# Optimization experiments

Hardware: AMD Instinct MI355X
Metric: run time of the kernel (lower is better)

## Reference

```python
import jax, jax.numpy as jnp
import numpy as np


def _gru_cell(x, h, W_ih, W_hh, b_ih, b_hh):
    # torch.nn.GRUCell semantics, gate order (r, z, n)
    gi = x @ W_ih.T + b_ih          # [B, 3H]
    gh = h @ W_hh.T + b_hh          # [B, 3H]
    ir, iz, inn = jnp.split(gi, 3, axis=-1)
    hr, hz, hn = jnp.split(gh, 3, axis=-1)
    r = jax.nn.sigmoid(ir + hr)
    z = jax.nn.sigmoid(iz + hz)
    n = jnp.tanh(inn + r * hn)
    return (1.0 - z) * n + z * h


def setup_inputs() -> dict:
    key = jax.random.key(0)
    ks = jax.random.split(key, 9)
    B, T, X, H = 128, 512, 64, 256
    s = 0.05
    return {
        "input": jax.random.normal(ks[0], (B, T, X), jnp.float32),
        "h_enc": jax.random.normal(ks[1], (B, H), jnp.float32),
        "W_ih": jax.random.normal(ks[2], (3 * H, X), jnp.float32) * s,
        "W_hh": jax.random.normal(ks[3], (3 * H, H), jnp.float32) * s,
        "b_ih": jnp.zeros((3 * H,), jnp.float32),
        "b_hh": jnp.zeros((3 * H,), jnp.float32),
        "W_out": jax.random.normal(ks[4], (X, H), jnp.float32) * s,
        "b_out": jnp.zeros((X,), jnp.float32),
        "mask0": jax.random.randint(ks[5], (T,), 0, 2, jnp.int32),
        "mask1": jax.random.randint(ks[6], (T,), 0, 2, jnp.int32),
        "skip_size": 4,
    }


def _skip_tables(T, skip):
    # Replicates Python-list negative indexing of the original forward.
    # Skip-list position at the GRU call (pre-append):  2i   if i<skip else i-skip
    # Skip-list position at the projection (post-append): 2i+1 if i<skip else i-skip
    # Positions < skip are zero placeholders; position p >= skip is H[p-skip].
    g_idx = np.zeros(T, np.int32); g_zero = np.zeros(T, bool)
    p_idx = np.zeros(T, np.int32); p_zero = np.zeros(T, bool)
    for i in range(T):
        pg = 2 * i if i < skip else i - skip
        pp = 2 * i + 1 if i < skip else i - skip
        g_zero[i] = pg < skip; g_idx[i] = max(pg - skip, 0)
        p_zero[i] = pp < skip; p_idx[i] = max(pp - skip, 0)
    return g_idx, g_zero, p_idx, p_zero


def reference(input, h_enc, W_ih, W_hh, b_ih, b_hh, W_out, b_out, mask0, mask1, skip_size):
    B, T, X = input.shape
    H = h_enc.shape[1]
    g_idx, g_zero, p_idx, p_zero = _skip_tables(T, int(skip_size))
    m0 = mask0.astype(input.dtype)
    m1 = mask1.astype(input.dtype)

    xs = (jnp.arange(T), m0, m1,
          jnp.asarray(g_idx), jnp.asarray(g_zero),
          jnp.asarray(p_idx), jnp.asarray(p_zero))

    def step(carry, sx):
        h_prev, x_prev, buf = carry          # buf: [T, B, H] history of GRU outputs
        i, a0, a1, gi, gz, pi, pz = sx
        skip_g = jnp.where(gz, 0.0, buf[gi])            # [B, H]
        hidden = h_prev * a0 + skip_g * a1
        h_new = _gru_cell(x_prev, hidden, W_ih, W_hh, b_ih, b_hh)
        buf = buf.at[i].set(h_new)                       # append H[i]
        skip_p = jnp.where(pz, 0.0, buf[pi])
        out = (h_prev + skip_p) @ W_out.T + b_out        # [B, X]
        return (h_new, out, buf), out

    buf0 = jnp.zeros((T, B, H), input.dtype)
    go = jnp.zeros((B, X), input.dtype)                  # GO token
    (_, _, _), outs = jax.lax.scan(step, (h_enc, go, buf0), xs)
    return jnp.transpose(outs, (1, 0, 2))                # [B, T, X]
```

## Files before the change

### kernel.cpp

```cpp
#include <hip/hip_runtime.h>

typedef _Float16 h2_t __attribute__((ext_vector_type(2)));

constexpr int T_ = 512;
constexpr int X_ = 64;
constexpr int H_ = 256;
constexpr int NWG = 128;
constexpr int NT = 512;
constexpr int RS = 16;

constexpr int G_TOTAL = 64 * NT;

__device__ __forceinline__ float sigmoid_f(float x) {
  float e = __expf(fminf(-x, 80.f));
  return 1.f / (1.f + e);
}
__device__ __forceinline__ float tanh_f(float x) {
  float e = __expf(fminf(-2.f * x, 80.f));
  return (1.f - e) / (1.f + e);
}

__device__ __forceinline__ unsigned pk2(float a, float b) {
  h2_t v;
  v[0] = (_Float16)a;
  v[1] = (_Float16)b;
  return __builtin_bit_cast(unsigned, v);
}
__device__ __forceinline__ uint4 pk8(const float* s) {
  return make_uint4(pk2(s[0], s[1]), pk2(s[2], s[3]), pk2(s[4], s[5]),
                    pk2(s[6], s[7]));
}

__device__ __forceinline__ float dotp(unsigned w, unsigned h, float acc) {
  h2_t wv = __builtin_bit_cast(h2_t, w);
  h2_t hv = __builtin_bit_cast(h2_t, h);
#if __has_builtin(__builtin_amdgcn_fdot2)
  return __builtin_amdgcn_fdot2(wv, hv, acc, false);
#else
  acc = fmaf((float)wv[0], (float)hv[0], acc);
  return fmaf((float)wv[1], (float)hv[1], acc);
#endif
}
__device__ __forceinline__ float dotq(uint4 w, uint4 h, float acc) {
  acc = dotp(w.x, h.x, acc);
  acc = dotp(w.y, h.y, acc);
  acc = dotp(w.z, h.z, acc);
  acc = dotp(w.w, h.w, acc);
  return acc;
}

__device__ __forceinline__ float dpp_xor1(float x) {
  int v = __builtin_amdgcn_update_dpp(0, __builtin_bit_cast(int, x), 0xB1,
                                      0xF, 0xF, true);
  return __builtin_bit_cast(float, v);
}
__device__ __forceinline__ float dpp_xor2(float x) {
  int v = __builtin_amdgcn_update_dpp(0, __builtin_bit_cast(int, x), 0x4E,
                                      0xF, 0xF, true);
  return __builtin_bit_cast(float, v);
}

__device__ __forceinline__ void bar_lds() {
  asm volatile("s_waitcnt lgkmcnt(0)\n\ts_barrier" ::: "memory");
}

__global__ void prep_kernel(const float* __restrict__ Wih,
                            const float* __restrict__ Whh,
                            const float* __restrict__ Wout,
                            uint4* __restrict__ G) {
  int id = blockIdx.x * 256 + threadIdx.x;
  if (id >= G_TOTAL) return;
  int t = id & (NT - 1), u = id >> 9;
  int c = t >> 1, kh = t & 1;
  if (u < 32) {
    int g = u >> 4, j = u & 15;
    G[id] = pk8(Whh + (size_t)(g * 256 + c) * H_ + kh * 128 + j * 8);
  } else if (u < 48) {
    int j = u - 32;
    G[id] = pk8(Whh + (size_t)(512 + c) * H_ + kh * 128 + j * 8);
  } else if (u < 60) {
    int v = u - 48, g = v >> 2, j = v & 3;
    G[id] = pk8(Wih + (size_t)(g * 256 + c) * X_ + kh * 32 + j * 8);
  } else {
    int j = u - 60, xc = t >> 3, sl = t & 7;
    G[id] = pk8(Wout + (size_t)xc * H_ + sl * 32 + j * 8);
  }
}

#define PTW(cp) (((cp) >> 4) * 36 + ((cp)&15))
#define HIW(w) ((w) + (((w) >> 6) << 2))


#define GATES(p, i, hn)                                                      \
  float hn;                                                                  \
  {                                                                          \
    float a0 = 0, a1 = 0, z0 = 0, z1 = 0, n0 = 0, n1 = 0, ni = 0;            \
    const uint4* h4 = ((const uint4*)hid2[p]) + kh * 17;                     \
    _Pragma("unroll") for (int j = 0; j < 16; j += 2) {                      \
      uint4 ha = h4[j], hb = h4[j + 1];       \
      uint4 wna = wn4[j * NT + t], wnb = wn4[(j + 1) * NT + t];              \
      a0 = dotq(whh_rz[j], ha, a0);                                          \
      a1 = dotq(whh_rz[j + 1], hb, a1);                                      \
      z0 = dotq(whh_rz[16 + j], ha, z0);                                     \
      z1 = dotq(whh_rz[17 + j], hb, z1);                                     \
      n0 = dotq(wna, ha, n0);                                                \
      n1 = dotq(wnb, hb, n1);                                                \
    }                                                                        \
    const uint4* x4 = ((const uint4*)xt2[p]) + kh * 4;                       \
    _Pragma("unroll") for (int j = 0; j < 4; ++j) {                          \
      uint4 xa = x4[j];                                                      \
      a0 = dotq(wih[j], xa, a0);                                             \
      z0 = dotq(wih[4 + j], xa, z0);                                         \
      ni = dotq(wih[8 + j], xa, ni);                                         \
    }                                                                        \
    float ar = a0 + a1, az = z0 + z1, anh = n0 + n1;                         \
    ar += dpp_xor1(ar);                                                      \
    az += dpp_xor1(az);                                                      \
    anh += dpp_xor1(anh);                                                    \
    ni += dpp_xor1(ni);                                                      \
    float r = sigmoid_f(ar + bsr);                                           \
    float z = sigmoid_f(az + bsz);                                           \
    float n = tanh_f(ni + bin_ + r * (anh + bhn_));                          \
    hn = fmaf(z, hid_reg - n, n);                    \
    if (kh == 0) ring[(i) & (RS - 1)][c] = hn;                               \
  }

#define PROJ_FIN(q, i)                                                       \
  {                                                                          \
    fa += dpp_xor1(fa);                                                      \
    fa += dpp_xor2(fa);                                                      \
    fa += __shfl_xor(fa, 4);                                                 \
    float o = fa + bo;                                                       \
    if (sl == 0) out[ob + (size_t)(i)*X_ + xc] = o;                          \
    float oo = __shfl_xor(o, 8);                                             \
    if ((t & 15) == 0) xt2[q][t >> 4] = pk2(o, oo);                          \
  }

#define PROJ(p, q, i)                                                        \
  {                                                                          \
    float fa = 0;                                                            \
    const uint4* p4 = (const uint4*)&pt2[p][sl * 36];                        \
    _Pragma("unroll") for (int j = 0; j < 4; ++j) fa =                       \
        dotq(wout[j], p4[j], fa);                                            \
    PROJ_FIN(q, i)                                                           \
  }

#define MSTEP(i, p, q)                                                       \
  {                                                                          \
    float fa = 0;                                                            \
    const uint4* p4 = (const uint4*)&pt2[p][sl * 36];                        \
    _Pragma("unroll") for (int j = 0; j < 4; ++j) fa =                       \
        dotq(wout[j], p4[j], fa);                                            \
    GATES(p, i, hn)                                                          \
    PROJ_FIN(q, i)                                                           \
    if ((i) + 1 < T_) {                                                      \
      float sgp = ring[((i) + 1 - 2 * skip) & (RS - 1)][c];                  \
      float hidn = m0f[(i) + 1] * hn + m1f[(i) + 1] * sgp;                   \
      float ptn = hn + sgp;                                                  \
      hid_reg = hidn;                                                        \
      float ho = dpp_xor2(hidn);                                             \
      float po = dpp_xor2(ptn);                                              \
      if ((t & 3) == 0) {                                                    \
        int w = t >> 2;                                                      \
        hid2[q][HIW(w)] = pk2(hidn, ho);                                     \
        pt2[q][PTW(w)] = pk2(ptn, po);                                       \
      }                                                                      \
    }                                                                        \
    bar_lds();                                                               \
  }

__global__ __attribute__((amdgpu_flat_work_group_size(NT, NT),
                          amdgpu_waves_per_eu(2, 2))) void decoder_kernel(
    const float* __restrict__ h_enc, const float* __restrict__ b_ih,
    const float* __restrict__ b_hh, const float* __restrict__ b_out,
    const int* __restrict__ mask0, const int* __restrict__ mask1,
    const int* __restrict__ skipp, const uint4* __restrict__ G,
    float* __restrict__ out) {
  __shared__ alignas(16) uint4 wn4[16 * NT];
  __shared__ float ring[RS][H_];
  __shared__ alignas(16) unsigned hid2[2][136];
  __shared__ alignas(16) unsigned pt2[2][8 * 36];
  __shared__ alignas(16) unsigned xt2[2][X_ / 2];
  __shared__ float m0f[T_], m1f[T_];

  const int t = threadIdx.x;
  const int b = blockIdx.x;
  const int c = t >> 1, kh = t & 1;
  const int xc = t >> 3, sl = t & 7;
  const size_t ob = (size_t)b * T_ * X_;

  uint4 whh_rz[32];
  uint4 wih[12];
  uint4 wout[4];
#pragma unroll
  for (int u = 0; u < 32; ++u) whh_rz[u] = G[u * NT + t];
#pragma unroll
  for (int u = 0; u < 12; ++u) wih[u] = G[(48 + u) * NT + t];
#pragma unroll
  for (int u = 0; u < 4; ++u) wout[u] = G[(60 + u) * NT + t];

#pragma unroll
  for (int u = 0; u < 16; ++u) wn4[u * NT + t] = G[(32 + u) * NT + t];
  m0f[t] = (float)mask0[t];
  m1f[t] = (float)mask1[t];

  const int skip = skipp[0];
  const int i0 = (skip == 0) ? T_ : ((2 * skip < T_) ? 2 * skip : T_);

  const float bsr = b_ih[c] + b_hh[c];
  const float bsz = b_ih[H_ + c] + b_hh[H_ + c];
  const float bin_ = b_ih[2 * H_ + c];
  const float bhn_ = b_hh[2 * H_ + c];
  const float bo = b_out[xc];

  float hp = h_enc[(size_t)b * H_ + c];
  float hid_reg = (float)mask0[0] * hp;
  float hps_reg = hp;
  {
    float ho = dpp_xor2(hid_reg);
    if ((t & 3) == 0) hid2[0][HIW(t >> 2)] = pk2(hid_reg, ho);
  }
  if (t < X_ / 2) xt2[0][t] = 0u;
  __syncthreads();

  for (int i = 0; i < i0; ++i) {
    const int p = i & 1, q = p ^ 1;
    GATES(p, i, hn)
    {
      int ppos = (i < skip) ? 2 * i + 1 : i - skip;
      bool pz = ppos < skip;
      int pi = ppos - skip;
      if (pi < 0) pi = 0;
      float sp = pz ? 0.f : ((pi == i) ? hn : ring[pi & (RS - 1)][c]);
      float ptv = hps_reg + sp;
      float po = dpp_xor2(ptv);
      if ((t & 3) == 0) pt2[p][PTW(t >> 2)] = pk2(ptv, po);
    }
    if (i + 1 < T_) {
      int i1 = i + 1;
      int pg = (i1 < skip) ? 2 * i1 : i1 - skip;
      bool gz = pg < skip;
      int gi = pg - skip;
      if (gi < 0) gi = 0;
      if (gi >= i1) gz = true;
      float sg = gz ? 0.f : ((gi == i) ? hn : ring[gi & (RS - 1)][c]);
      float hidn = m0f[i1] * hn + m1f[i1] * sg;
      hid_reg = hidn;
      float ho = dpp_xor2(hidn);
      if ((t & 3) == 0) hid2[q][HIW(t >> 2)] = pk2(hidn, ho);
      if (skip > 0 && i1 >= 2 * skip) {
        float sgp = ring[(i1 - 2 * skip) & (RS - 1)][c];
        float ptn = hn + sgp;
        float po2 = dpp_xor2(ptn);
        if ((t & 3) == 0) pt2[q][PTW(t >> 2)] = pk2(ptn, po2);
      }
    }
    hps_reg = hn;
    __syncthreads();
    PROJ(p, q, i)
    __syncthreads();
  }

#pragma unroll 1
  for (int i = i0; i < T_; i += 2) {
    MSTEP(i, 0, 1)
    MSTEP(i + 1, 1, 0)
  }
}

extern "C" void kernel_launch(void* const* d_in, const int* in_sizes, int n_in,
                              void* d_out, int out_size, void* d_ws,
                              size_t ws_size, hipStream_t stream) {
  (void)in_sizes; (void)n_in; (void)out_size; (void)ws_size;
  const float* h_enc = (const float*)d_in[1];
  const float* W_ih = (const float*)d_in[2];
  const float* W_hh = (const float*)d_in[3];
  const float* b_ih = (const float*)d_in[4];
  const float* b_hh = (const float*)d_in[5];
  const float* W_out = (const float*)d_in[6];
  const float* b_out = (const float*)d_in[7];
  const int* mask0 = (const int*)d_in[8];
  const int* mask1 = (const int*)d_in[9];
  const int* skipp = (const int*)d_in[10];
  float* out = (float*)d_out;
  uint4* G = (uint4*)d_ws;

  prep_kernel<<<dim3(G_TOTAL / 256), dim3(256), 0, stream>>>(W_ih, W_hh,
                                                             W_out, G);
  decoder_kernel<<<dim3(NWG), dim3(NT), 0, stream>>>(
      h_enc, b_ih, b_hh, b_out, mask0, mask1, skipp, G, out);
}
```

Baseline: 1.077 ms.

## Remap GRU work so each thread quad computes two hidden columns

Each group of four threads now owns two adjacent hidden columns and splits K four ways, instead of each pair of threads owning one column with K split two ways. The weight packing, the LDS layouts for hidden, x and projection vectors, and the reductions change to match. The packed fp16 pairs are now two columns from one thread, so the dpp exchange before LDS writes goes away and each hidden vector load feeds six dot chains. The cost is an extra dpp step in each reduction, eight reductions per thread instead of four, and more per-thread gate math.

Measured after the change: 1.219 ms. +13.2%, slower.

```diff
diff --git a/kernel.cpp b/kernel.cpp
--- a/kernel.cpp
+++ b/kernel.cpp
@@ -59,6 +59,9 @@
                                       0xF, 0xF, true);
   return __builtin_bit_cast(float, v);
 }
+#define QRED(v)       \
+  v += dpp_xor1(v);   \
+  v += dpp_xor2(v);
 
 __device__ __forceinline__ void bar_lds() {
   asm volatile("s_waitcnt lgkmcnt(0)\n\ts_barrier" ::: "memory");
@@ -71,58 +74,67 @@
   int id = blockIdx.x * 256 + threadIdx.x;
   if (id >= G_TOTAL) return;
   int t = id & (NT - 1), u = id >> 9;
-  int c = t >> 1, kh = t & 1;
+  int cp = t >> 2, kq = t & 3, c0 = 2 * cp;
   if (u < 32) {
-    int g = u >> 4, j = u & 15;
-    G[id] = pk8(Whh + (size_t)(g * 256 + c) * H_ + kh * 128 + j * 8);
+    int g = u >> 4, col01 = (u >> 3) & 1, j = u & 7;
+    G[id] = pk8(Whh + (size_t)(g * 256 + c0 + col01) * H_ + kq * 64 + j * 8);
   } else if (u < 48) {
-    int j = u - 32;
-    G[id] = pk8(Whh + (size_t)(512 + c) * H_ + kh * 128 + j * 8);
+    int v = u - 32, col01 = v >> 3, j = v & 7;
+    G[id] = pk8(Whh + (size_t)(512 + c0 + col01) * H_ + kq * 64 + j * 8);
   } else if (u < 60) {
-    int v = u - 48, g = v >> 2, j = v & 3;
-    G[id] = pk8(Wih + (size_t)(g * 256 + c) * X_ + kh * 32 + j * 8);
+    int v = u - 48, g = v >> 2, col01 = (v >> 1) & 1, j = v & 1;
+    G[id] = pk8(Wih + (size_t)(g * 256 + c0 + col01) * X_ + kq * 16 + j * 8);
   } else {
     int j = u - 60, xc = t >> 3, sl = t & 7;
     G[id] = pk8(Wout + (size_t)xc * H_ + sl * 32 + j * 8);
   }
 }
 
-#define PTW(cp) (((cp) >> 4) * 36 + ((cp)&15))
-#define HIW(w) ((w) + (((w) >> 6) << 2))
-
-
-#define GATES(p, i, hn)                                                      \
-  float hn;                                                                  \
+
+#define GATES(p, i, hnA, hnB)                                                \
+  float hnA, hnB;                                                            \
   {                                                                          \
-    float a0 = 0, a1 = 0, z0 = 0, z1 = 0, n0 = 0, n1 = 0, ni = 0;            \
-    const uint4* h4 = ((const uint4*)hid2[p]) + kh * 17;                     \
-    _Pragma("unroll") for (int j = 0; j < 16; j += 2) {                      \
-      uint4 ha = h4[j], hb = h4[j + 1];       \
-      uint4 wna = wn4[j * NT + t], wnb = wn4[(j + 1) * NT + t];              \
-      a0 = dotq(whh_rz[j], ha, a0);                                          \
-      a1 = dotq(whh_rz[j + 1], hb, a1);                                      \
-      z0 = dotq(whh_rz[16 + j], ha, z0);                                     \
-      z1 = dotq(whh_rz[17 + j], hb, z1);                                     \
-      n0 = dotq(wna, ha, n0);                                                \
-      n1 = dotq(wnb, hb, n1);                                                \
+    float arA = 0, arB = 0, azA = 0, azB = 0, anA = 0, anB = 0;              \
+    float niA = 0, niB = 0;                                                  \
+    const uint4* h4 = ((const uint4*)hid4[p]) + kq * 9;                      \
+    _Pragma("unroll") for (int j = 0; j < 8; ++j) {                          \
+      uint4 hj = h4[j];                                                      \
+      uint4 wnA = wn_l[j * NT + t], wnB = wn_l[(8 + j) * NT + t];            \
+      arA = dotq(whh_rz[j], hj, arA);                                        \
+      arB = dotq(whh_rz[8 + j], hj, arB);                                    \
+      azA = dotq(whh_rz[16 + j], hj, azA);                                   \
+      azB = dotq(whh_rz[24 + j], hj, azB);                                   \
+      anA = dotq(wnA, hj, anA);                                              \
+      anB = dotq(wnB, hj, anB);                                              \
     }                                                                        \
-    const uint4* x4 = ((const uint4*)xt2[p]) + kh * 4;                       \
-    _Pragma("unroll") for (int j = 0; j < 4; ++j) {                          \
-      uint4 xa = x4[j];                                                      \
-      a0 = dotq(wih[j], xa, a0);                                             \
-      z0 = dotq(wih[4 + j], xa, z0);                                         \
-      ni = dotq(wih[8 + j], xa, ni);                                         \
+    const uint4* x4 = ((const uint4*)xt4[p]) + kq * 3;                       \
+    uint4 xa = x4[0], xb = x4[1];                                            \
+    arA = dotq(wih[0], xa, arA);                                             \
+    arA = dotq(wih[1], xb, arA);                                             \
+    arB = dotq(wih[2], xa, arB);                                             \
+    arB = dotq(wih[3], xb, arB);                                             \
+    azA = dotq(wih[4], xa, azA);                                             \
+    azA = dotq(wih[5], xb, azA);                                             \
+    azB = dotq(wih[6], xa, azB);                                             \
+    azB = dotq(wih[7], xb, azB);                                             \
+    niA = dotq(wih[8], xa, niA);                                             \
+    niA = dotq(wih[9], xb, niA);                                             \
+    niB = dotq(wih[10], xa, niB);                                            \
+    niB = dotq(wih[11], xb, niB);                                            \
+    QRED(arA) QRED(arB) QRED(azA) QRED(azB)                                  \
+    QRED(anA) QRED(anB) QRED(niA) QRED(niB)                                  \
+    float rA = sigmoid_f(arA + bsrA);                                        \
+    float zA = sigmoid_f(azA + bszA);                                        \
+    float nA = tanh_f(niA + binA + rA * (anA + bhnA));                       \
+    hnA = fmaf(zA, hidA - nA, nA);                                           \
+    float rB = sigmoid_f(arB + bsrB);                                        \
+    float zB = sigmoid_f(azB + bszB);                                        \
+    float nB = tanh_f(niB + binB + rB * (anB + bhnB));                       \
+    hnB = fmaf(zB, hidB - nB, nB);                                           \
+    if (kq == 0) {                                                           \
+      ring[(i) & (RS - 1)][c0] = hnA;                                        \
+      ring[(i) & (RS - 1)][c0 + 1] = hnB;                                    \
     }                                                                        \
-    float ar = a0 + a1, az = z0 + z1, anh = n0 + n1;                         \
-    ar += dpp_xor1(ar);                                                      \
-    az += dpp_xor1(az);                                                      \
-    anh += dpp_xor1(anh);                                                    \
-    ni += dpp_xor1(ni);                                                      \
-    float r = sigmoid_f(ar + bsr);                                           \
-    float z = sigmoid_f(az + bsz);                                           \
-    float n = tanh_f(ni + bin_ + r * (anh + bhn_));                          \
-    hn = fmaf(z, hid_reg - n, n);                    \
-    if (kh == 0) ring[(i) & (RS - 1)][c] = hn;                               \
   }
 
 #define PROJ_FIN(q, i)                                                       \
@@ -133,7 +145,8 @@
     float o = fa + bo;                                                       \
     if (sl == 0) out[ob + (size_t)(i)*X_ + xc] = o;                          \
     float oo = __shfl_xor(o, 8);                                             \
-    if ((t & 15) == 0) xt2[q][t >> 4] = pk2(o, oo);                          \
+    if ((t & 15) == 0)                                                       \
+      ((unsigned*)xt4[q])[(xc >> 4) * 12 + ((xc & 15) >> 1)] = pk2(o, oo);   \
   }
 
 #define PROJ(p, q, i)                                                        \
@@ -151,19 +164,20 @@
     const uint4* p4 = (const uint4*)&pt2[p][sl * 36];                        \
     _Pragma("unroll") for (int j = 0; j < 4; ++j) fa =                       \
         dotq(wout[j], p4[j], fa);                                            \
-    GATES(p, i, hn)                                                          \
+    GATES(p, i, hnA, hnB)                                                    \
     PROJ_FIN(q, i)                                                           \
     if ((i) + 1 < T_) {                                                      \
-      float sgp = ring[((i) + 1 - 2 * skip) & (RS - 1)][c];                  \
-      float hidn = m0f[(i) + 1] * hn + m1f[(i) + 1] * sgp;                   \
-      float ptn = hn + sgp;                                                  \
-      hid_reg = hidn;                                                        \
-      float ho = dpp_xor2(hidn);                                             \
-      float po = dpp_xor2(ptn);                                              \
-      if ((t & 3) == 0) {                                                    \
-        int w = t >> 2;                                                      \
-        hid2[q][HIW(w)] = pk2(hidn, ho);                                     \
-        pt2[q][PTW(w)] = pk2(ptn, po);                                       \
+      int ri = ((i) + 1 - 2 * skip) & (RS - 1);                              \
+      float sgA = ring[ri][c0], sgB = ring[ri][c0 + 1];                      \
+      float m0v = m0f[(i) + 1], m1v = m1f[(i) + 1];                          \
+      float hidnA = fmaf(m0v, hnA, m1v * sgA);                               \
+      float hidnB = fmaf(m0v, hnB, m1v * sgB);                               \
+      hidA = hidnA;                                                          \
+      hidB = hidnB;                                                          \
+      if (kq == 0) {                                                         \
+        ((unsigned*)hid4[q])[(cp >> 5) * 36 + (cp & 31)] =                   \
+            pk2(hidnA, hidnB);                                               \
+        pt2[q][(cp >> 4) * 36 + (cp & 15)] = pk2(hnA + sgA, hnB + sgB);      \
       }                                                                      \
     }                                                                        \
     bar_lds();                                                               \
@@ -176,16 +190,17 @@
     const int* __restrict__ mask0, const int* __restrict__ mask1,
     const int* __restrict__ skipp, const uint4* __restrict__ G,
     float* __restrict__ out) {
-  __shared__ alignas(16) uint4 wn4[16 * NT];
+  __shared__ alignas(16) uint4 wn_l[16 * NT];
   __shared__ float ring[RS][H_];
-  __shared__ alignas(16) unsigned hid2[2][136];
+  __shared__ alignas(16) unsigned hid4[2][144];
   __shared__ alignas(16) unsigned pt2[2][8 * 36];
-  __shared__ alignas(16) unsigned xt2[2][X_ / 2];
+  __shared__ alignas(16) unsigned xt4[2][48];
   __shared__ float m0f[T_], m1f[T_];
 
   const int t = threadIdx.x;
   const int b = blockIdx.x;
-  const int c = t >> 1, kh = t & 1;
+  const int cp = t >> 2, kq = t & 3;
+  const int c0 = 2 * cp;
   const int xc = t >> 3, sl = t & 7;
   const size_t ob = (size_t)b * T_ * X_;
 
@@ -200,41 +215,57 @@
   for (int u = 0; u < 4; ++u) wout[u] = G[(60 + u) * NT + t];
 
 #pragma unroll
-  for (int u = 0; u < 16; ++u) wn4[u * NT + t] = G[(32 + u) * NT + t];
+  for (int u = 0; u < 16; ++u) wn_l[u * NT + t] = G[(32 + u) * NT + t];
   m0f[t] = (float)mask0[t];
   m1f[t] = (float)mask1[t];
 
   const int skip = skipp[0];
   const int i0 = (skip == 0) ? T_ : ((2 * skip < T_) ? 2 * skip : T_);
 
-  const float bsr = b_ih[c] + b_hh[c];
-  const float bsz = b_ih[H_ + c] + b_hh[H_ + c];
-  const float bin_ = b_ih[2 * H_ + c];
-  const float bhn_ = b_hh[2 * H_ + c];
+  const float bsrA = b_ih[c0] + b_hh[c0];
+  const float bsrB = b_ih[c0 + 1] + b_hh[c0 + 1];
+  const float bszA = b_ih[H_ + c0] + b_hh[H_ + c0];
+  const float bszB = b_ih[H_ + c0 + 1] + b_hh[H_ + c0 + 1];
+  const float binA = b_ih[2 * H_ + c0];
+  const float binB = b_ih[2 * H_ + c0 + 1];
+  const float bhnA = b_hh[2 * H_ + c0];
+  const float bhnB = b_hh[2 * H_ + c0 + 1];
   const float bo = b_out[xc];
 
-  float hp = h_enc[(size_t)b * H_ + c];
-  float hid_reg = (float)mask0[0] * hp;
-  float hps_reg = hp;
-  {
-    float ho = dpp_xor2(hid_reg);
-    if ((t & 3) == 0) hid2[0][HIW(t >> 2)] = pk2(hid_reg, ho);
-  }
-  if (t < X_ / 2) xt2[0][t] = 0u;
+  float hpA = h_enc[(size_t)b * H_ + c0];
+  float hpB = h_enc[(size_t)b * H_ + c0 + 1];
+  const float m00 = (float)mask0[0];
+  float hidA = m00 * hpA, hidB = m00 * hpB;
+  float hpsA = hpA, hpsB = hpB;
+  if (kq == 0) {
+    ring[RS - 1][c0] = hpA;
+    ring[RS - 1][c0 + 1] = hpB;
+    ((unsigned*)hid4[0])[(cp >> 5) * 36 + (cp & 31)] = pk2(hidA, hidB);
+  }
+  if (t < 48) ((unsigned*)xt4[0])[t] = 0u;
   __syncthreads();
 
   for (int i = 0; i < i0; ++i) {
     const int p = i & 1, q = p ^ 1;
-    GATES(p, i, hn)
+    GATES(p, i, hnA, hnB)
     {
       int ppos = (i < skip) ? 2 * i + 1 : i - skip;
       bool pz = ppos < skip;
       int pi = ppos - skip;
       if (pi < 0) pi = 0;
-      float sp = pz ? 0.f : ((pi == i) ? hn : ring[pi & (RS - 1)][c]);
-      float ptv = hps_reg + sp;
-      float po = dpp_xor2(ptv);
-      if ((t & 3) == 0) pt2[p][PTW(t >> 2)] = pk2(ptv, po);
+      float spA, spB;
+      if (pz) {
+        spA = 0.f;
+        spB = 0.f;
+      } else if (pi == i) {
+        spA = hnA;
+        spB = hnB;
+      } else {
+        spA = ring[pi & (RS - 1)][c0];
+        spB = ring[pi & (RS - 1)][c0 + 1];
+      }
+      if (kq == 0)
+        pt2[p][(cp >> 4) * 36 + (cp & 15)] = pk2(hpsA + spA, hpsB + spB);
     }
     if (i + 1 < T_) {
       int i1 = i + 1;
@@ -243,19 +274,32 @@
       int gi = pg - skip;
       if (gi < 0) gi = 0;
       if (gi >= i1) gz = true;
-      float sg = gz ? 0.f : ((gi == i) ? hn : ring[gi & (RS - 1)][c]);
-      float hidn = m0f[i1] * hn + m1f[i1] * sg;
-      hid_reg = hidn;
-      float ho = dpp_xor2(hidn);
-      if ((t & 3) == 0) hid2[q][HIW(t >> 2)] = pk2(hidn, ho);
+      float sgA, sgB;
+      if (gz) {
+        sgA = 0.f;
+        sgB = 0.f;
+      } else if (gi == i) {
+        sgA = hnA;
+        sgB = hnB;
+      } else {
+        sgA = ring[gi & (RS - 1)][c0];
+        sgB = ring[gi & (RS - 1)][c0 + 1];
+      }
+      float hidnA = m0f[i1] * hnA + m1f[i1] * sgA;
+      float hidnB = m0f[i1] * hnB + m1f[i1] * sgB;
+      hidA = hidnA;
+      hidB = hidnB;
+      if (kq == 0)
+        ((unsigned*)hid4[q])[(cp >> 5) * 36 + (cp & 31)] = pk2(hidnA, hidnB);
       if (skip > 0 && i1 >= 2 * skip) {
-        float sgp = ring[(i1 - 2 * skip) & (RS - 1)][c];
-        float ptn = hn + sgp;
-        float po2 = dpp_xor2(ptn);
-        if ((t & 3) == 0) pt2[q][PTW(t >> 2)] = pk2(ptn, po2);
+        int ri = (i1 - 2 * skip) & (RS - 1);
+        float sgpA = ring[ri][c0], sgpB = ring[ri][c0 + 1];
+        if (kq == 0)
+          pt2[q][(cp >> 4) * 36 + (cp & 15)] = pk2(hnA + sgpA, hnB + sgpB);
       }
     }
-    hps_reg = hn;
+    hpsA = hnA;
+    hpsB = hnB;
     __syncthreads();
     PROJ(p, q, i)
     __syncthreads();
```

## Process two batch rows per workgroup to reuse register-resident weights

Applied to the files above, without the earlier changes.

Each workgroup now handles two batch elements (A and B) at once, halving the grid to 64 workgroups. Every weight fragment loaded from registers or LDS is applied to both hidden states, which amortizes the LDS weight reads and adds independent dot-product chains to hide latency. The skip ring buffer now holds both rows' hidden values as packed fp16 pairs, so skip values are stored at reduced precision. The cost is twice the arithmetic per step on each workgroup and fewer workgroups active in parallel.

Measured after the change: 1.900 ms. 1.76x slower.

```diff
diff --git a/kernel.cpp b/kernel.cpp
--- a/kernel.cpp
+++ b/kernel.cpp
@@ -5,7 +5,7 @@
 constexpr int T_ = 512;
 constexpr int X_ = 64;
 constexpr int H_ = 256;
-constexpr int NWG = 128;
+constexpr int NWG = 64;
 constexpr int NT = 512;
 constexpr int RS = 16;
 
@@ -91,79 +91,105 @@
 #define HIW(w) ((w) + (((w) >> 6) << 2))
 
 
-#define GATES(p, i, hn)                                                      \
-  float hn;                                                                  \
+#define GATES2(p, i, hnA, hnB)                                               \
+  float hnA, hnB;                                                            \
   {                                                                          \
-    float a0 = 0, a1 = 0, z0 = 0, z1 = 0, n0 = 0, n1 = 0, ni = 0;            \
-    const uint4* h4 = ((const uint4*)hid2[p]) + kh * 17;                     \
-    _Pragma("unroll") for (int j = 0; j < 16; j += 2) {                      \
-      uint4 ha = h4[j], hb = h4[j + 1];       \
-      uint4 wna = wn4[j * NT + t], wnb = wn4[(j + 1) * NT + t];              \
-      a0 = dotq(whh_rz[j], ha, a0);                                          \
-      a1 = dotq(whh_rz[j + 1], hb, a1);                                      \
-      z0 = dotq(whh_rz[16 + j], ha, z0);                                     \
-      z1 = dotq(whh_rz[17 + j], hb, z1);                                     \
-      n0 = dotq(wna, ha, n0);                                                \
-      n1 = dotq(wnb, hb, n1);                                                \
-    }                                                                        \
-    const uint4* x4 = ((const uint4*)xt2[p]) + kh * 4;                       \
+    float arA = 0, azA = 0, anA = 0, niA = 0;                                \
+    float arB = 0, azB = 0, anB = 0, niB = 0;                                \
+    const uint4* hA4 = ((const uint4*)hid2A[p]) + kh * 17;                   \
+    const uint4* hB4 = ((const uint4*)hid2B[p]) + kh * 17;                   \
+    _Pragma("unroll") for (int j = 0; j < 16; ++j) {                         \
+      uint4 hA = hA4[j], hB = hB4[j];                 \
+      uint4 wn = wn4[j * NT + t];                \
+      arA = dotq(whh_rz[j], hA, arA);                                        \
+      arB = dotq(whh_rz[j], hB, arB);                                        \
+      azA = dotq(whh_rz[16 + j], hA, azA);                                   \
+      azB = dotq(whh_rz[16 + j], hB, azB);                                   \
+      anA = dotq(wn, hA, anA);                                               \
+      anB = dotq(wn, hB, anB);                                               \
+    }                                                                        \
+    const uint4* xA4 = ((const uint4*)xtA[p]) + kh * 4;                      \
+    const uint4* xB4 = ((const uint4*)xtB[p]) + kh * 4;                      \
     _Pragma("unroll") for (int j = 0; j < 4; ++j) {                          \
-      uint4 xa = x4[j];                                                      \
-      a0 = dotq(wih[j], xa, a0);                                             \
-      z0 = dotq(wih[4 + j], xa, z0);                                         \
-      ni = dotq(wih[8 + j], xa, ni);                                         \
-    }                                                                        \
-    float ar = a0 + a1, az = z0 + z1, anh = n0 + n1;                         \
-    ar += dpp_xor1(ar);                                                      \
-    az += dpp_xor1(az);                                                      \
-    anh += dpp_xor1(anh);                                                    \
-    ni += dpp_xor1(ni);                                                      \
-    float r = sigmoid_f(ar + bsr);                                           \
-    float z = sigmoid_f(az + bsz);                                           \
-    float n = tanh_f(ni + bin_ + r * (anh + bhn_));                          \
-    hn = fmaf(z, hid_reg - n, n);                    \
-    if (kh == 0) ring[(i) & (RS - 1)][c] = hn;                               \
-  }
-
-#define PROJ_FIN(q, i)                                                       \
+      uint4 xa = xA4[j], xb = xB4[j];                                        \
+      arA = dotq(wih[j], xa, arA);                                           \
+      arB = dotq(wih[j], xb, arB);                                           \
+      azA = dotq(wih[4 + j], xa, azA);                                       \
+      azB = dotq(wih[4 + j], xb, azB);                                       \
+      niA = dotq(wih[8 + j], xa, niA);                                       \
+      niB = dotq(wih[8 + j], xb, niB);                                       \
+    }                                                                        \
+    arA += dpp_xor1(arA);                                                    \
+    azA += dpp_xor1(azA);                                                    \
+    anA += dpp_xor1(anA);                                                    \
+    niA += dpp_xor1(niA);                                                    \
+    arB += dpp_xor1(arB);                                                    \
+    azB += dpp_xor1(azB);                                                    \
+    anB += dpp_xor1(anB);                                                    \
+    niB += dpp_xor1(niB);                                                    \
+    float rA = sigmoid_f(arA + bsr), zA = sigmoid_f(azA + bsz);              \
+    float nA = tanh_f(niA + bin_ + rA * (anA + bhn_));                       \
+    hnA = fmaf(zA, hidA - nA, nA);                                           \
+    float rB = sigmoid_f(arB + bsr), zB = sigmoid_f(azB + bsz);              \
+    float nB = tanh_f(niB + bin_ + rB * (anB + bhn_));                       \
+    hnB = fmaf(zB, hidB - nB, nB);                                           \
+    if (kh == 0) ringAB[(i) & (RS - 1)][c] = pk2(hnA, hnB);                  \
+  }
+
+#define PROJ_DOTS(p)                                                         \
+  float faA = 0, faB = 0;                                                    \
   {                                                                          \
-    fa += dpp_xor1(fa);                                                      \
-    fa += dpp_xor2(fa);                                                      \
-    fa += __shfl_xor(fa, 4);                                                 \
-    float o = fa + bo;                                                       \
-    if (sl == 0) out[ob + (size_t)(i)*X_ + xc] = o;                          \
-    float oo = __shfl_xor(o, 8);                                             \
-    if ((t & 15) == 0) xt2[q][t >> 4] = pk2(o, oo);                          \
-  }
-
-#define PROJ(p, q, i)                                                        \
+    const uint4* pA4 = (const uint4*)&pt2A[p][sl * 36];                      \
+    const uint4* pB4 = (const uint4*)&pt2B[p][sl * 36];                      \
+    _Pragma("unroll") for (int j = 0; j < 4; ++j) {                          \
+      faA = dotq(wout[j], pA4[j], faA);                                      \
+      faB = dotq(wout[j], pB4[j], faB);                                      \
+    }                                                                        \
+  }
+
+#define PROJ_FIN2(q, i)                                                      \
   {                                                                          \
-    float fa = 0;                                                            \
-    const uint4* p4 = (const uint4*)&pt2[p][sl * 36];                        \
-    _Pragma("unroll") for (int j = 0; j < 4; ++j) fa =                       \
-        dotq(wout[j], p4[j], fa);                                            \
-    PROJ_FIN(q, i)                                                           \
-  }
-
-#define MSTEP(i, p, q)                                                       \
+    faA += dpp_xor1(faA);                                                    \
+    faA += dpp_xor2(faA);                                                    \
+    faA += __shfl_xor(faA, 4);                                               \
+    faB += dpp_xor1(faB);                                                    \
+    faB += dpp_xor2(faB);                                                    \
+    faB += __shfl_xor(faB, 4);                                               \
+    float oA = faA + bo, oB = faB + bo;                                      \
+    if (sl == 0) {                                                           \
+      out[obA + (size_t)(i)*X_ + xc] = oA;                                   \
+      out[obB + (size_t)(i)*X_ + xc] = oB;                                   \
+    }                                                                        \
+    float ooA = __shfl_xor(oA, 8), ooB = __shfl_xor(oB, 8);                  \
+    if ((t & 15) == 0) {                                                     \
+      xtA[q][t >> 4] = pk2(oA, ooA);                                         \
+      xtB[q][t >> 4] = pk2(oB, ooB);                                         \
+    }                                                                        \
+  }
+
+#define MSTEP2(i, p, q)                                                      \
   {                                                                          \
-    float fa = 0;                                                            \
-    const uint4* p4 = (const uint4*)&pt2[p][sl * 36];                        \
-    _Pragma("unroll") for (int j = 0; j < 4; ++j) fa =                       \
-        dotq(wout[j], p4[j], fa);                                            \
-    GATES(p, i, hn)                                                          \
-    PROJ_FIN(q, i)                                                           \
+    PROJ_DOTS(p)                                                             \
+    GATES2(p, i, hnA, hnB)                                                   \
+    PROJ_FIN2(q, i)                                                          \
     if ((i) + 1 < T_) {                                                      \
-      float sgp = ring[((i) + 1 - 2 * skip) & (RS - 1)][c];                  \
-      float hidn = m0f[(i) + 1] * hn + m1f[(i) + 1] * sgp;                   \
-      float ptn = hn + sgp;                                                  \
-      hid_reg = hidn;                                                        \
-      float ho = dpp_xor2(hidn);                                             \
-      float po = dpp_xor2(ptn);                                              \
+      unsigned rw = ringAB[((i) + 1 - 2 * skip) & (RS - 1)][c];              \
+      h2_t rv = __builtin_bit_cast(h2_t, rw);                                \
+      float sgA = (float)rv[0], sgB = (float)rv[1];                          \
+      float m0v = m0f[(i) + 1], m1v = m1f[(i) + 1];                          \
+      float hidnA = fmaf(m0v, hnA, m1v * sgA);                               \
+      float hidnB = fmaf(m0v, hnB, m1v * sgB);                               \
+      float ptnA = hnA + sgA, ptnB = hnB + sgB;                              \
+      hidA = hidnA;                                                          \
+      hidB = hidnB;                                                          \
+      float hoA = dpp_xor2(hidnA), poA = dpp_xor2(ptnA);                     \
+      float hoB = dpp_xor2(hidnB), poB = dpp_xor2(ptnB);                     \
       if ((t & 3) == 0) {                                                    \
         int w = t >> 2;                                                      \
-        hid2[q][HIW(w)] = pk2(hidn, ho);                                     \
-        pt2[q][PTW(w)] = pk2(ptn, po);                                       \
+        hid2A[q][HIW(w)] = pk2(hidnA, hoA);                                  \
+        pt2A[q][PTW(w)] = pk2(ptnA, poA);                                    \
+        hid2B[q][HIW(w)] = pk2(hidnB, hoB);                                  \
+        pt2B[q][PTW(w)] = pk2(ptnB, poB);                                    \
       }                                                                      \
     }                                                                        \
     bar_lds();                                                               \
@@ -177,17 +203,21 @@
     const int* __restrict__ skipp, const uint4* __restrict__ G,
     float* __restrict__ out) {
   __shared__ alignas(16) uint4 wn4[16 * NT];
-  __shared__ float ring[RS][H_];
-  __shared__ alignas(16) unsigned hid2[2][136];
-  __shared__ alignas(16) unsigned pt2[2][8 * 36];
-  __shared__ alignas(16) unsigned xt2[2][X_ / 2];
+  __shared__ alignas(16) unsigned ringAB[RS][H_];
+  __shared__ alignas(16) unsigned hid2A[2][136];
+  __shared__ alignas(16) unsigned hid2B[2][136];
+  __shared__ alignas(16) unsigned pt2A[2][8 * 36];
+  __shared__ alignas(16) unsigned pt2B[2][8 * 36];
+  __shared__ alignas(16) unsigned xtA[2][X_ / 2];
+  __shared__ alignas(16) unsigned xtB[2][X_ / 2];
   __shared__ float m0f[T_], m1f[T_];
 
   const int t = threadIdx.x;
-  const int b = blockIdx.x;
+  const int bA = 2 * blockIdx.x, bB = bA + 1;
   const int c = t >> 1, kh = t & 1;
   const int xc = t >> 3, sl = t & 7;
-  const size_t ob = (size_t)b * T_ * X_;
+  const size_t obA = (size_t)bA * T_ * X_;
+  const size_t obB = (size_t)bB * T_ * X_;
 
   uint4 whh_rz[32];
   uint4 wih[12];
@@ -213,28 +243,50 @@
   const float bhn_ = b_hh[2 * H_ + c];
   const float bo = b_out[xc];
 
-  float hp = h_enc[(size_t)b * H_ + c];
-  float hid_reg = (float)mask0[0] * hp;
-  float hps_reg = hp;
+  float hpA = h_enc[(size_t)bA * H_ + c];
+  float hpB = h_enc[(size_t)bB * H_ + c];
+  const float m00 = (float)mask0[0];
+  float hidA = m00 * hpA, hidB = m00 * hpB;
+  float hpsA = hpA, hpsB = hpB;
   {
-    float ho = dpp_xor2(hid_reg);
-    if ((t & 3) == 0) hid2[0][HIW(t >> 2)] = pk2(hid_reg, ho);
-  }
-  if (t < X_ / 2) xt2[0][t] = 0u;
+    float hoA = dpp_xor2(hidA), hoB = dpp_xor2(hidB);
+    if ((t & 3) == 0) {
+      hid2A[0][HIW(t >> 2)] = pk2(hidA, hoA);
+      hid2B[0][HIW(t >> 2)] = pk2(hidB, hoB);
+    }
+  }
+  if (t < X_ / 2) {
+    xtA[0][t] = 0u;
+    xtB[0][t] = 0u;
+  }
   __syncthreads();
 
   for (int i = 0; i < i0; ++i) {
     const int p = i & 1, q = p ^ 1;
-    GATES(p, i, hn)
+    GATES2(p, i, hnA, hnB)
     {
       int ppos = (i < skip) ? 2 * i + 1 : i - skip;
       bool pz = ppos < skip;
       int pi = ppos - skip;
       if (pi < 0) pi = 0;
-      float sp = pz ? 0.f : ((pi == i) ? hn : ring[pi & (RS - 1)][c]);
-      float ptv = hps_reg + sp;
-      float po = dpp_xor2(ptv);
-      if ((t & 3) == 0) pt2[p][PTW(t >> 2)] = pk2(ptv, po);
+      float spA, spB;
+      if (pz) {
+        spA = 0.f;
+        spB = 0.f;
+      } else if (pi == i) {
+        spA = hnA;
+        spB = hnB;
+      } else {
+        h2_t rv = __builtin_bit_cast(h2_t, ringAB[pi & (RS - 1)][c]);
+        spA = (float)rv[0];
+        spB = (float)rv[1];
+      }
+      float ptvA = hpsA + spA, ptvB = hpsB + spB;
+      float poA = dpp_xor2(ptvA), poB = dpp_xor2(ptvB);
+      if ((t & 3) == 0) {
+        pt2A[p][PTW(t >> 2)] = pk2(ptvA, poA);
+        pt2B[p][PTW(t >> 2)] = pk2(ptvB, poB);
+      }
     }
     if (i + 1 < T_) {
       int i1 = i + 1;
@@ -243,28 +295,51 @@
       int gi = pg - skip;
       if (gi < 0) gi = 0;
       if (gi >= i1) gz = true;
-      float sg = gz ? 0.f : ((gi == i) ? hn : ring[gi & (RS - 1)][c]);
-      float hidn = m0f[i1] * hn + m1f[i1] * sg;
-      hid_reg = hidn;
-      float ho = dpp_xor2(hidn);
-      if ((t & 3) == 0) hid2[q][HIW(t >> 2)] = pk2(hidn, ho);
+      float sgA, sgB;
+      if (gz) {
+        sgA = 0.f;
+        sgB = 0.f;
+      } else if (gi == i) {
+        sgA = hnA;
+        sgB = hnB;
+      } else {
+        h2_t rv = __builtin_bit_cast(h2_t, ringAB[gi & (RS - 1)][c]);
+        sgA = (float)rv[0];
+        sgB = (float)rv[1];
+      }
+      float hidnA = m0f[i1] * hnA + m1f[i1] * sgA;
+      float hidnB = m0f[i1] * hnB + m1f[i1] * sgB;
+      hidA = hidnA;
+      hidB = hidnB;
+      float hoA = dpp_xor2(hidnA), hoB = dpp_xor2(hidnB);
+      if ((t & 3) == 0) {
+        hid2A[q][HIW(t >> 2)] = pk2(hidnA, hoA);
+        hid2B[q][HIW(t >> 2)] = pk2(hidnB, hoB);
+      }
       if (skip > 0 && i1 >= 2 * skip) {
-        float sgp = ring[(i1 - 2 * skip) & (RS - 1)][c];
-        float ptn = hn + sgp;
-        float po2 = dpp_xor2(ptn);
-        if ((t & 3) == 0) pt2[q][PTW(t >> 2)] = pk2(ptn, po2);
+        h2_t rv = __builtin_bit_cast(h2_t, ringAB[(i1 - 2 * skip) & (RS - 1)][c]);
+        float ptnA = hnA + (float)rv[0], ptnB = hnB + (float)rv[1];
+        float poA = dpp_xor2(ptnA), poB = dpp_xor2(ptnB);
+        if ((t & 3) == 0) {
+          pt2A[q][PTW(t >> 2)] = pk2(ptnA, poA);
+          pt2B[q][PTW(t >> 2)] = pk2(ptnB, poB);
+        }
       }
     }
-    hps_reg = hn;
+    hpsA = hnA;
+    hpsB = hnB;
     __syncthreads();
-    PROJ(p, q, i)
+    {
+      PROJ_DOTS(p)
+      PROJ_FIN2(q, i)
+    }
     __syncthreads();
   }
 
 #pragma unroll 1
   for (int i = i0; i < T_; i += 2) {
-    MSTEP(i, 0, 1)
-    MSTEP(i + 1, 1, 0)
+    MSTEP2(i, 0, 1)
+    MSTEP2(i + 1, 1, 0)
   }
 }
 
```

## Accumulate GRU gate dot products in packed fp16 FMA with parity-ordered phases

Applied to the files above, without the earlier changes.

Replaces the fp32-accumulating fdot2 dot products with packed half2 FMAs that accumulate in fp16 across four partial accumulators, reduced to fp32 at the end. This halves the per-element instruction pressure, since each packed FMA does two MACs without a separate reduction dependency. Odd and even waves also run the projection and gate phases in opposite order, to stagger LDS and VALU use across waves. The risk is lower numerical precision from fp16 accumulation over 256-long dot products inside a 512-step recurrence, where errors can compound.

After: 1.164 ms. 8.0% more time.

```diff
diff --git a/kernel.cpp b/kernel.cpp
--- a/kernel.cpp
+++ b/kernel.cpp
@@ -41,12 +41,31 @@
   return fmaf((float)wv[1], (float)hv[1], acc);
 #endif
 }
-__device__ __forceinline__ float dotq(uint4 w, uint4 h, float acc) {
-  acc = dotp(w.x, h.x, acc);
-  acc = dotp(w.y, h.y, acc);
-  acc = dotp(w.z, h.z, acc);
-  acc = dotp(w.w, h.w, acc);
-  return acc;
+
+__device__ __forceinline__ h2_t pkfma(unsigned w, unsigned h, h2_t acc) {
+  h2_t wv = __builtin_bit_cast(h2_t, w);
+  h2_t hv = __builtin_bit_cast(h2_t, h);
+#if __has_builtin(__builtin_elementwise_fma)
+  return __builtin_elementwise_fma(wv, hv, acc);
+#else
+  return wv * hv + acc;
+#endif
+}
+#define PKQ(W4, H4, A)                                                      \
+  do {                                                                      \
+    A[0] = pkfma((W4).x, (H4).x, A[0]);                                     \
+    A[1] = pkfma((W4).y, (H4).y, A[1]);                                     \
+    A[2] = pkfma((W4).z, (H4).z, A[2]);                                     \
+    A[3] = pkfma((W4).w, (H4).w, A[3]);                                     \
+  } while (0)
+
+#define ONE2U 0x3C003C00u
+
+__device__ __forceinline__ float pks(const h2_t* A) {
+  h2_t s0 = A[0] + A[1];
+  h2_t s1 = A[2] + A[3];
+  float f = dotp(__builtin_bit_cast(unsigned, s0), ONE2U, 0.f);
+  return dotp(__builtin_bit_cast(unsigned, s1), ONE2U, f);
 }
 
 __device__ __forceinline__ float dpp_xor1(float x) {
@@ -91,29 +110,27 @@
 #define HIW(w) ((w) + (((w) >> 6) << 2))
 
 
-#define GATES(p, i, hn)                                                      \
-  float hn;                                                                  \
+#define GATES_BODY(p, i)                                                     \
   {                                                                          \
-    float a0 = 0, a1 = 0, z0 = 0, z1 = 0, n0 = 0, n1 = 0, ni = 0;            \
+    h2_t Z2 = (h2_t)0;                                                       \
+    h2_t AR[4] = {Z2, Z2, Z2, Z2}, AZ[4] = {Z2, Z2, Z2, Z2};                 \
+    h2_t AN[4] = {Z2, Z2, Z2, Z2}, NI[4] = {Z2, Z2, Z2, Z2};                 \
     const uint4* h4 = ((const uint4*)hid2[p]) + kh * 17;                     \
-    _Pragma("unroll") for (int j = 0; j < 16; j += 2) {                      \
-      uint4 ha = h4[j], hb = h4[j + 1];       \
-      uint4 wna = wn4[j * NT + t], wnb = wn4[(j + 1) * NT + t];              \
-      a0 = dotq(whh_rz[j], ha, a0);                                          \
-      a1 = dotq(whh_rz[j + 1], hb, a1);                                      \
-      z0 = dotq(whh_rz[16 + j], ha, z0);                                     \
-      z1 = dotq(whh_rz[17 + j], hb, z1);                                     \
-      n0 = dotq(wna, ha, n0);                                                \
-      n1 = dotq(wnb, hb, n1);                                                \
+    _Pragma("unroll") for (int j = 0; j < 16; ++j) {                         \
+      uint4 hj = h4[j];                       \
+      uint4 wn = wn4[j * NT + t];                                            \
+      PKQ(whh_rz[j], hj, AR);                                                \
+      PKQ(whh_rz[16 + j], hj, AZ);                                           \
+      PKQ(wn, hj, AN);                                                       \
     }                                                                        \
     const uint4* x4 = ((const uint4*)xt2[p]) + kh * 4;                       \
     _Pragma("unroll") for (int j = 0; j < 4; ++j) {                          \
       uint4 xa = x4[j];                                                      \
-      a0 = dotq(wih[j], xa, a0);                                             \
-      z0 = dotq(wih[4 + j], xa, z0);                                         \
-      ni = dotq(wih[8 + j], xa, ni);                                         \
-    }                                                                        \
-    float ar = a0 + a1, az = z0 + z1, anh = n0 + n1;                         \
+      PKQ(wih[j], xa, AR);                                                   \
+      PKQ(wih[4 + j], xa, AZ);                                               \
+      PKQ(wih[8 + j], xa, NI);                                               \
+    }                                                                        \
+    float ar = pks(AR), az = pks(AZ), anh = pks(AN), ni = pks(NI);           \
     ar += dpp_xor1(ar);                                                      \
     az += dpp_xor1(az);                                                      \
     anh += dpp_xor1(anh);                                                    \
@@ -125,6 +142,17 @@
     if (kh == 0) ring[(i) & (RS - 1)][c] = hn;                               \
   }
 
+#define PROJ_DOTS_BODY(p)                                                    \
+  {                                                                          \
+    h2_t Z2 = (h2_t)0;                                                       \
+    h2_t FA[4] = {Z2, Z2, Z2, Z2};                                           \
+    const uint4* p4 = (const uint4*)&pt2[p][sl * 36];                        \
+    _Pragma("unroll") for (int j = 0; j < 4; ++j) {                          \
+      PKQ(wout[j], p4[j], FA);                                               \
+    }                                                                        \
+    fa = pks(FA);                                                            \
+  }
+
 #define PROJ_FIN(q, i)                                                       \
   {                                                                          \
     fa += dpp_xor1(fa);                                                      \
@@ -136,22 +164,16 @@
     if ((t & 15) == 0) xt2[q][t >> 4] = pk2(o, oo);                          \
   }
 
-#define PROJ(p, q, i)                                                        \
-  {                                                                          \
-    float fa = 0;                                                            \
-    const uint4* p4 = (const uint4*)&pt2[p][sl * 36];                        \
-    _Pragma("unroll") for (int j = 0; j < 4; ++j) fa =                       \
-        dotq(wout[j], p4[j], fa);                                            \
-    PROJ_FIN(q, i)                                                           \
-  }
-
 #define MSTEP(i, p, q)                                                       \
   {                                                                          \
-    float fa = 0;                                                            \
-    const uint4* p4 = (const uint4*)&pt2[p][sl * 36];                        \
-    _Pragma("unroll") for (int j = 0; j < 4; ++j) fa =                       \
-        dotq(wout[j], p4[j], fa);                                            \
-    GATES(p, i, hn)                                                          \
+    float hn, fa;                                                            \
+    if (weven) {                                                             \
+      PROJ_DOTS_BODY(p)                                                      \
+      GATES_BODY(p, i)                                                       \
+    } else {                                                                 \
+      GATES_BODY(p, i)                                                       \
+      PROJ_DOTS_BODY(p)                                                      \
+    }                                                                        \
     PROJ_FIN(q, i)                                                           \
     if ((i) + 1 < T_) {                                                      \
       float sgp = ring[((i) + 1 - 2 * skip) & (RS - 1)][c];                  \
@@ -187,6 +209,7 @@
   const int b = blockIdx.x;
   const int c = t >> 1, kh = t & 1;
   const int xc = t >> 3, sl = t & 7;
+  const bool weven = ((t >> 6) & 1) == 0;
   const size_t ob = (size_t)b * T_ * X_;
 
   uint4 whh_rz[32];
@@ -225,7 +248,8 @@
 
   for (int i = 0; i < i0; ++i) {
     const int p = i & 1, q = p ^ 1;
-    GATES(p, i, hn)
+    float hn, fa;
+    GATES_BODY(p, i)
     {
       int ppos = (i < skip) ? 2 * i + 1 : i - skip;
       bool pz = ppos < skip;
@@ -257,7 +281,8 @@
     }
     hps_reg = hn;
     __syncthreads();
-    PROJ(p, q, i)
+    PROJ_DOTS_BODY(p)
+    PROJ_FIN(q, i)
     __syncthreads();
   }
 
```
